# Optimization experiments

Hardware: AMD Instinct MI355X
Metric: run time of the kernel (lower is better)

## Reference

```python
import jax, jax.numpy as jnp
import numpy as np

DIM = 1024
N_HEADS = 16
HEAD_DIM = DIM // N_HEADS
HIDDEN = 4 * DIM
B, T = 4, 2048
EPS = 1e-5


def setup_inputs() -> dict:
    key = jax.random.key(0)
    ks = jax.random.split(key, 12)
    s = lambda fan_in: 1.0 / np.sqrt(fan_in)
    return {
        "x": jax.random.normal(ks[0], (B, T, DIM), jnp.float32),
        "ln1_g": jnp.ones((DIM,), jnp.float32),
        "ln1_b": jnp.zeros((DIM,), jnp.float32),
        "qkv_w": jax.random.normal(ks[1], (DIM, 3 * DIM), jnp.float32) * s(DIM),
        "qkv_b": jnp.zeros((3 * DIM,), jnp.float32),
        "proj_w": jax.random.normal(ks[2], (DIM, DIM), jnp.float32) * s(DIM),
        "proj_b": jnp.zeros((DIM,), jnp.float32),
        "ln2_g": jnp.ones((DIM,), jnp.float32),
        "ln2_b": jnp.zeros((DIM,), jnp.float32),
        "ff1_w": jax.random.normal(ks[3], (DIM, HIDDEN), jnp.float32) * s(DIM),
        "ff1_b": jnp.zeros((HIDDEN,), jnp.float32),
        "ff2_w": jax.random.normal(ks[4], (HIDDEN, DIM), jnp.float32) * s(HIDDEN),
        "ff2_b": jnp.zeros((DIM,), jnp.float32),
    }


def _layernorm(x, g, b):
    mu = jnp.mean(x, axis=-1, keepdims=True)
    var = jnp.mean(jnp.square(x - mu), axis=-1, keepdims=True)
    return (x - mu) * jax.lax.rsqrt(var + EPS) * g + b


def _attn(x, qkv_w, qkv_b, proj_w, proj_b):
    Bx, Tx, C = x.shape
    qkv = (x @ qkv_w + qkv_b).reshape(Bx, Tx, 3, N_HEADS, HEAD_DIM)
    q, k, v = (qkv[:, :, i].transpose(0, 2, 1, 3) for i in range(3))  # [B,H,T,hd]
    att = jnp.einsum('bhqd,bhkd->bhqk', q, k) / np.sqrt(HEAD_DIM)
    causal = jnp.tril(jnp.ones((Tx, Tx), bool))
    att = jnp.where(causal, att, -jnp.inf)
    att = jax.nn.softmax(att, axis=-1)
    out = jnp.einsum('bhqk,bhkd->bhqd', att, v).transpose(0, 2, 1, 3).reshape(Bx, Tx, C)
    return out @ proj_w + proj_b


def reference(x, ln1_g, ln1_b, qkv_w, qkv_b, proj_w, proj_b,
              ln2_g, ln2_b, ff1_w, ff1_b, ff2_w, ff2_b):
    x = x + _attn(_layernorm(x, ln1_g, ln1_b), qkv_w, qkv_b, proj_w, proj_b)
    h = _layernorm(x, ln2_g, ln2_b)
    h = jax.nn.gelu(h @ ff1_w + ff1_b, approximate=False) @ ff2_w + ff2_b
    return x + h
```

## Files before the change

### kernel.cpp

```cpp
#include <hip/hip_runtime.h>
#include <hip/hip_bf16.h>
#include <math.h>

#define DIM 1024
#define NHEADS 16
#define HD 64
#define TT 2048
#define BB 4
#define MTOK (BB*TT)
#define HID 4096

typedef __attribute__((ext_vector_type(8))) short bf16x8;
typedef __attribute__((ext_vector_type(4))) float f32x4;
typedef unsigned short u16;
typedef unsigned int u32;

__device__ inline u16 f2b(float f){
  __hip_bfloat16 h = __float2bfloat16(f);
  return __builtin_bit_cast(u16, h);
}

__device__ inline void load_lds16(const void* g, void* l){
  __builtin_amdgcn_global_load_lds(
      (const __attribute__((address_space(1))) void*)g,
      (__attribute__((address_space(3))) void*)l,
      16, 0, 0);
}

__global__ __launch_bounds__(256) void wconv_t(const float* __restrict__ W,
                                               u16* __restrict__ Wt, int K, int N){
  __shared__ float tl[32][33];
  const int k0 = blockIdx.x*32, n0 = blockIdx.y*32;
  const int tx = threadIdx.x & 31, ty = threadIdx.x >> 5;
  #pragma unroll
  for (int r=0;r<32;r+=8)
    tl[ty+r][tx] = W[(size_t)(k0+ty+r)*N + (n0+tx)];
  __syncthreads();
  #pragma unroll
  for (int r=0;r<32;r+=8)
    Wt[(size_t)(n0+ty+r)*K + (k0+tx)] = f2b(tl[tx][ty+r]);
}

__global__ __launch_bounds__(256) void ln_fwd(const float* __restrict__ x,
                                              const float* __restrict__ g,
                                              const float* __restrict__ bta,
                                              u16* __restrict__ out){
  const int row = blockIdx.x, t = threadIdx.x;
  const float4 v = ((const float4*)(x + (size_t)row*DIM))[t];
  float s  = v.x+v.y+v.z+v.w;
  float s2 = v.x*v.x+v.y*v.y+v.z*v.z+v.w*v.w;
  #pragma unroll
  for (int m=1;m<64;m<<=1){ s += __shfl_xor(s,m); s2 += __shfl_xor(s2,m); }
  __shared__ float red[8];
  if ((t&63)==0){ red[t>>6]=s; red[4+(t>>6)]=s2; }
  __syncthreads();
  s  = red[0]+red[1]+red[2]+red[3];
  s2 = red[4]+red[5]+red[6]+red[7];
  const float mu = s*(1.0f/DIM);
  const float rstd = rsqrtf(s2*(1.0f/DIM) - mu*mu + 1e-5f);
  const float4 gv = ((const float4*)g)[t];
  const float4 bv = ((const float4*)bta)[t];
  ushort4 ov;
  ov.x = f2b((v.x-mu)*rstd*gv.x + bv.x);
  ov.y = f2b((v.y-mu)*rstd*gv.y + bv.y);
  ov.z = f2b((v.z-mu)*rstd*gv.z + bv.z);
  ov.w = f2b((v.w-mu)*rstd*gv.w + bv.w);
  ((ushort4*)out)[(size_t)row*(DIM/4) + t] = ov;
}

template<int EPI>
__global__ __launch_bounds__(256) void gemm_bt(
    const u16* __restrict__ A, const u16* __restrict__ Bt,
    const float* __restrict__ bias, const float* __restrict__ resid,
    float* __restrict__ outf, u16* __restrict__ outh,
    u16* __restrict__ qo, u16* __restrict__ ko, u16* __restrict__ vo,
    int M, int N, int K)
{
  __shared__ __align__(16) u16 smem[16384];
  u16* As = smem;
  u16* Bs = smem + 8192;
  u16* Ct = smem;
  const int t = threadIdx.x, wv = t>>6, ln = t&63;
  const int nbx = gridDim.x, nwg = nbx*gridDim.y;
  const int bid = blockIdx.y*nbx + blockIdx.x;
  const int cpx = nwg>>3;
  const int wid = (bid&7)*cpx + (bid>>3);
  const int m0 = (wid/nbx)*128, n0 = (wid%nbx)*128;
  const int wr = wv>>1, wc = wv&1;
  const int hi = ln>>4, lr = hi*4, lc = ln&15;
  f32x4 acc[4][4] = {};

  int rdoff[2][2];
  #pragma unroll
  for (int kk=0; kk<2; kk++)
    rdoff[kk][0] = ((kk*4 + hi) ^ (lc&7)) << 3;

  for (int kt=0; kt<K; kt+=64){
    #pragma unroll
    for (int j=0;j<4;j++){
      const int chunk = j*256 + t;
      const int row = chunk>>3;
      const int cS  = (chunk&7) ^ (row&7);
      load_lds16(A  + (size_t)(m0+row)*K + kt + cS*8, (char*)As + chunk*16);
      load_lds16(Bt + (size_t)(n0+row)*K + kt + cS*8, (char*)Bs + chunk*16);
    }
    asm volatile("s_waitcnt vmcnt(0)" ::: "memory");
    __syncthreads();
    bf16x8 af[4][2], bfr[4][2];
    #pragma unroll
    for (int mi=0;mi<4;mi++){
      const int rbase = (wr*64 + mi*16 + lc) << 6;
      af[mi][0] = *(const bf16x8*)&As[rbase + rdoff[0][0]];
      af[mi][1] = *(const bf16x8*)&As[rbase + rdoff[1][0]];
    }
    #pragma unroll
    for (int ni=0;ni<4;ni++){
      const int rbase = (wc*64 + ni*16 + lc) << 6;
      bfr[ni][0] = *(const bf16x8*)&Bs[rbase + rdoff[0][0]];
      bfr[ni][1] = *(const bf16x8*)&Bs[rbase + rdoff[1][0]];
    }
    #pragma unroll
    for (int kk=0;kk<2;kk++)
      #pragma unroll
      for (int mi=0;mi<4;mi++)
        #pragma unroll
        for (int ni=0;ni<4;ni++)
          acc[mi][ni] = __builtin_amdgcn_mfma_f32_16x16x32_bf16(af[mi][kk], bfr[ni][kk], acc[mi][ni], 0,0,0);
    __syncthreads();
  }

  if constexpr (EPI==1 || EPI==3){
    #pragma unroll
    for (int ni=0;ni<4;ni++){
      const int gn = n0 + wc*64 + ni*16 + lc;
      const float bv = bias[gn];
      #pragma unroll
      for (int mi=0;mi<4;mi++){
        const int gmb = m0 + wr*64 + mi*16 + lr;
        f32x4 a = acc[mi][ni];
        #pragma unroll
        for (int i=0;i<4;i++){
          const size_t idx = (size_t)(gmb+i)*DIM + gn;
          outf[idx] = a[i] + bv + resid[idx];
        }
      }
    }
  } else {
    const int part = (EPI==0) ? (n0>>10) : 0;
    #pragma unroll
    for (int ni=0;ni<4;ni++){
      const int gn = n0 + wc*64 + ni*16 + lc;
      const float bv = bias[gn];
      const int cl = wc*64 + ni*16 + lc;
      #pragma unroll
      for (int mi=0;mi<4;mi++){
        f32x4 a = acc[mi][ni];
        #pragma unroll
        for (int i=0;i<4;i++){
          const int rl = wr*64 + mi*16 + lr + i;
          float val = a[i] + bv;
          if constexpr (EPI==2)
            val = 0.5f*val*(1.0f + erff(val*0.70710678118654752f));
          int r, c;
          if (EPI==0 && part==2){ r = cl; c = rl; } else { r = rl; c = cl; }
          const int chunk = c>>3;
          const int csw = (chunk&8) | ((chunk ^ (r&7)) & 7);
          Ct[(r<<7) + (csw<<3) + (c&7)] = f2b(val);
        }
      }
    }
    __syncthreads();
    const int cid = t & 7, rsub = t >> 3;
    const int bb = m0>>11, tok0b = m0&2047;
    const int h0 = (EPI==0) ? ((n0&1023)>>6) : 0;
    #pragma unroll
    for (int pass=0; pass<4; ++pass){
      const int rr = pass*32 + rsub;
      #pragma unroll
      for (int hh=0; hh<2; ++hh){
        const int chunk = hh*8 + cid;
        const int sw = (chunk&8) | ((chunk ^ (rr&7)) & 7);
        const bf16x8 vvv = *(const bf16x8*)&Ct[(rr<<7) + (sw<<3)];
        if constexpr (EPI==2){
          *(bf16x8*)&outh[(size_t)(m0+rr)*HID + n0 + chunk*8] = vvv;
        } else {
          if (part==2){
            const int head = h0 + (rr>>6), d = rr&63;
            *(bf16x8*)&vo[(((size_t)bb*NHEADS + head)*HD + d)*TT + tok0b + chunk*8] = vvv;
          } else {
            u16* dst = part ? ko : qo;
            const int head = h0 + hh;
            *(bf16x8*)&dst[(((size_t)bb*NHEADS + head)*TT + tok0b + rr)*HD + cid*8] = vvv;
          }
        }
      }
    }
  }
}

__global__ __launch_bounds__(512) void attn_fwd(
    const u16* __restrict__ qpt, const u16* __restrict__ kb, const u16* __restrict__ vtb,
    u16* __restrict__ o)
{
  __shared__ __align__(16) u16 Kd[2][64*64];
  __shared__ __align__(16) u16 Vd[2][64*64];
  __shared__ __align__(16) u32 Ps[8][16*40];
  const int t = threadIdx.x, wv = t>>6, ln = t&63;
  const int bid  = blockIdx.y*gridDim.x + blockIdx.x;
  const int orig = (bid&7)*128 + (bid>>3);
  const int bh   = orig>>4;
  const int qb   = 15 - (orig&15);
  const size_t base = (size_t)bh*TT*HD;
  const int hi = ln>>4, lc = ln&15;
  const int nt = 2*qb + 2;
  const int qbase = qb*128 + wv*16;
  const int qrow  = qbase + lc;

  const bf16x8 qf0 = *(const bf16x8*)(qpt + base + (size_t)qrow*HD + hi*8);
  const bf16x8 qf1 = *(const bf16x8*)(qpt + base + (size_t)qrow*HD + 32 + hi*8);
  f32x4 oacc[4] = {};
  float mrun = -1e30f, lrun = 0.f;
  const float SCQ = 0.125f * 1.44269504f;
  u32* pw = Ps[wv];

  const int srow = t>>3;
  const int sch  = t&7;
  const int gch  = (sch ^ (srow&7))<<3;

  auto STAGE = [&](int nb, int kt){
    load_lds16(kb  + base + (size_t)(kt*64+srow)*HD + gch, &Kd[nb][srow*64 + sch*8]);
    load_lds16(vtb + base + (size_t)srow*TT + kt*64 + gch, &Vd[nb][srow*64 + sch*8]);
  };
  auto FRAG = [&](const u16* buf, int r, int ch)->bf16x8{
    return *(const bf16x8*)(buf + r*64 + ((ch ^ (r&7))<<3));
  };

  int cur = 0;
  STAGE(0, 0);
  asm volatile("s_waitcnt vmcnt(0)" ::: "memory");
  __syncthreads();

  for (int kt=0; kt<nt; kt++){
    if (kt+1 < nt) STAGE(cur^1, kt+1);
    const u16* Kb = Kd[cur];
    const u16* Vb = Vd[cur];
    if (kt*64 <= qbase + 15){
      float p[4][4];
      float mx = -1e30f;
      __builtin_amdgcn_s_setprio(1);
      #pragma unroll
      for (int cf=0;cf<4;cf++){
        const int r = cf*16 + lc;
        const bf16x8 kf0 = FRAG(Kb, r, hi);
        const bf16x8 kf1 = FRAG(Kb, r, hi+4);
        f32x4 z = {0.f,0.f,0.f,0.f};
        z = __builtin_amdgcn_mfma_f32_16x16x32_bf16(kf0, qf0, z, 0,0,0);
        z = __builtin_amdgcn_mfma_f32_16x16x32_bf16(kf1, qf1, z, 0,0,0);
        p[cf][0]=z[0]; p[cf][1]=z[1]; p[cf][2]=z[2]; p[cf][3]=z[3];
      }
      __builtin_amdgcn_s_setprio(0);
      if (kt*64 + 63 > qbase){
        #pragma unroll
        for (int cf=0;cf<4;cf++)
          #pragma unroll
          for (int i=0;i<4;i++){
            const int kvg = kt*64 + cf*16 + 4*hi + i;
            float sv = p[cf][i]*SCQ;
            sv = (kvg > qrow) ? -1e30f : sv;
            p[cf][i] = sv;
            mx = fmaxf(mx, sv);
          }
      } else {
        #pragma unroll
        for (int cf=0;cf<4;cf++)
          #pragma unroll
          for (int i=0;i<4;i++){
            const float sv = p[cf][i]*SCQ;
            p[cf][i] = sv;
            mx = fmaxf(mx, sv);
          }
      }
      mx = fmaxf(mx, __shfl_xor(mx, 16));
      mx = fmaxf(mx, __shfl_xor(mx, 32));
      if (__any(mx > mrun + 11.0f)){
        const float mnew = fmaxf(mrun, mx);
        const float sc = exp2f(mrun - mnew);
        mrun = mnew;
        lrun *= sc;
        const float s0 = __shfl(sc, 4*hi+0);
        const float s1 = __shfl(sc, 4*hi+1);
        const float s2 = __shfl(sc, 4*hi+2);
        const float s3 = __shfl(sc, 4*hi+3);
        #pragma unroll
        for (int df=0;df<4;df++){
          oacc[df][0] *= s0; oacc[df][1] *= s1;
          oacc[df][2] *= s2; oacc[df][3] *= s3;
        }
      }
      float ssum = 0.f;
      #pragma unroll
      for (int cf=0;cf<4;cf++)
        #pragma unroll
        for (int i=0;i<4;i++){
          const float pv = exp2f(p[cf][i] - mrun);
          p[cf][i] = pv;
          ssum += pv;
        }
      ssum += __shfl_xor(ssum, 16);
      ssum += __shfl_xor(ssum, 32);
      lrun += ssum;
      #pragma unroll
      for (int cf=0;cf<4;cf++){
        uint2 wpk;
        wpk.x = (u32)f2b(p[cf][0]) | ((u32)f2b(p[cf][1])<<16);
        wpk.y = (u32)f2b(p[cf][2]) | ((u32)f2b(p[cf][3])<<16);
        *(uint2*)&pw[lc*40 + cf*8 + 2*hi] = wpk;
      }
      asm volatile("s_waitcnt lgkmcnt(0)" ::: "memory");
      __builtin_amdgcn_sched_barrier(0);
      const bf16x8 paA = *(const bf16x8*)&pw[lc*40 + 4*hi];
      const bf16x8 paB = *(const bf16x8*)&pw[lc*40 + 16 + 4*hi];
      __builtin_amdgcn_s_setprio(1);
      #pragma unroll
      for (int df=0;df<4;df++){
        const bf16x8 v0 = FRAG(Vb, df*16+lc, hi);
        const bf16x8 v1 = FRAG(Vb, df*16+lc, hi+4);
        oacc[df] = __builtin_amdgcn_mfma_f32_16x16x32_bf16(paA, v0, oacc[df], 0,0,0);
        oacc[df] = __builtin_amdgcn_mfma_f32_16x16x32_bf16(paB, v1, oacc[df], 0,0,0);
      }
      __builtin_amdgcn_s_setprio(0);
    }
    asm volatile("s_waitcnt vmcnt(0)" ::: "memory");
    __syncthreads();
    cur ^= 1;
  }

  const int b = bh>>4, h = bh&15;
  const float l0 = __shfl(lrun, 4*hi+0);
  const float l1 = __shfl(lrun, 4*hi+1);
  const float l2 = __shfl(lrun, 4*hi+2);
  const float l3 = __shfl(lrun, 4*hi+3);
  const float inv[4] = {1.0f/l0, 1.0f/l1, 1.0f/l2, 1.0f/l3};
  const int qg0 = qbase + 4*hi;
  #pragma unroll
  for (int i=0;i<4;i++){
    const size_t rowb = ((size_t)b*TT + (size_t)(qg0 + i))*DIM + h*HD;
    #pragma unroll
    for (int df=0;df<4;df++)
      o[rowb + df*16 + lc] = f2b(oacc[df][i]*inv[i]);
  }
}

extern "C" void kernel_launch(void* const* d_in, const int* in_sizes, int n_in,
                              void* d_out, int out_size, void* d_ws, size_t ws_size,
                              hipStream_t stream){
  (void)in_sizes; (void)n_in; (void)out_size; (void)ws_size;
  const float* x     = (const float*)d_in[0];
  const float* ln1g  = (const float*)d_in[1];
  const float* ln1b  = (const float*)d_in[2];
  const float* qkvw  = (const float*)d_in[3];
  const float* qkvb  = (const float*)d_in[4];
  const float* projw = (const float*)d_in[5];
  const float* projb = (const float*)d_in[6];
  const float* ln2g  = (const float*)d_in[7];
  const float* ln2b  = (const float*)d_in[8];
  const float* ff1w  = (const float*)d_in[9];
  const float* ff1b  = (const float*)d_in[10];
  const float* ff2w  = (const float*)d_in[11];
  const float* ff2b  = (const float*)d_in[12];
  float* out = (float*)d_out;

  char* ws = (char*)d_ws;
  size_t off = 0;
  auto alloc = [&](size_t n){ char* p = ws + off; off += (n + 255) & ~(size_t)255; return p; };
  u16* wqkvt  = (u16*)alloc((size_t)3072*1024*2);
  u16* wprojt = (u16*)alloc((size_t)1024*1024*2);
  u16* wff1t  = (u16*)alloc((size_t)4096*1024*2);
  u16* wff2t  = (u16*)alloc((size_t)1024*4096*2);
  u16* h1     = (u16*)alloc((size_t)MTOK*DIM*2);
  u16* qbuf   = (u16*)alloc((size_t)MTOK*DIM*2);
  u16* kbuf   = (u16*)alloc((size_t)MTOK*DIM*2);
  u16* vbuf   = (u16*)alloc((size_t)MTOK*DIM*2);
  u16* aout   = (u16*)alloc((size_t)MTOK*DIM*2);
  float* x2   = (float*)alloc((size_t)MTOK*DIM*4);
  u16* h2     = (u16*)alloc((size_t)MTOK*DIM*2);
  u16* act    = (u16*)alloc((size_t)MTOK*HID*2);

  wconv_t<<<dim3(1024/32, 3072/32), 256, 0, stream>>>(qkvw, wqkvt, 1024, 3072);
  wconv_t<<<dim3(1024/32, 1024/32), 256, 0, stream>>>(projw, wprojt, 1024, 1024);
  wconv_t<<<dim3(1024/32, 4096/32), 256, 0, stream>>>(ff1w, wff1t, 1024, 4096);
  wconv_t<<<dim3(4096/32, 1024/32), 256, 0, stream>>>(ff2w, wff2t, 4096, 1024);

  ln_fwd<<<MTOK, 256, 0, stream>>>(x, ln1g, ln1b, h1);

  gemm_bt<0><<<dim3(3072/128, MTOK/128), 256, 0, stream>>>(
      h1, wqkvt, qkvb, nullptr, nullptr, nullptr, qbuf, kbuf, vbuf, MTOK, 3072, 1024);

  attn_fwd<<<dim3(TT/128, BB*NHEADS), 512, 0, stream>>>(qbuf, kbuf, vbuf, aout);

  gemm_bt<1><<<dim3(1024/128, MTOK/128), 256, 0, stream>>>(
      aout, wprojt, projb, x, x2, nullptr, nullptr, nullptr, nullptr, MTOK, 1024, 1024);

  ln_fwd<<<MTOK, 256, 0, stream>>>(x2, ln2g, ln2b, h2);

  gemm_bt<2><<<dim3(4096/128, MTOK/128), 256, 0, stream>>>(
      h2, wff1t, ff1b, nullptr, nullptr, act, nullptr, nullptr, nullptr, MTOK, HID, 1024);

  gemm_bt<3><<<dim3(1024/128, MTOK/128), 256, 0, stream>>>(
      act, wff2t, ff2b, x2, out, nullptr, nullptr, nullptr, nullptr, MTOK, DIM, HID);
}
```

Baseline: 481.0 us.

## Double-buffer GEMM LDS tiles with BK=32 to overlap loads and MFMA

Restructures the GEMM main loop so K steps by 32, with two LDS buffers: the next tile's global→LDS loads are issued before computing on the current buffer, and one barrier per iteration replaces two. The XOR swizzle on the LDS layout is dropped in favour of a plain row-major 32-column layout. A barrier is added before the epilogue reuses shared memory. The smaller K tile doubles the iteration count and the unswizzled reads may cause LDS bank conflicts.

New measurement: 492.3 us. 1.02x slower.

```diff
diff --git a/kernel.cpp b/kernel.cpp
--- a/kernel.cpp
+++ b/kernel.cpp
@@ -77,8 +77,6 @@
     int M, int N, int K)
 {
   __shared__ __align__(16) u16 smem[16384];
-  u16* As = smem;
-  u16* Bs = smem + 8192;
   u16* Ct = smem;
   const int t = threadIdx.x, wv = t>>6, ln = t&63;
   const int nbx = gridDim.x, nwg = nbx*gridDim.y;
@@ -90,44 +88,49 @@
   const int hi = ln>>4, lr = hi*4, lc = ln&15;
   f32x4 acc[4][4] = {};
 
-  int rdoff[2][2];
-  #pragma unroll
-  for (int kk=0; kk<2; kk++)
-    rdoff[kk][0] = ((kk*4 + hi) ^ (lc&7)) << 3;
-
-  for (int kt=0; kt<K; kt+=64){
-    #pragma unroll
-    for (int j=0;j<4;j++){
-      const int chunk = j*256 + t;
-      const int row = chunk>>3;
-      const int cS  = (chunk&7) ^ (row&7);
-      load_lds16(A  + (size_t)(m0+row)*K + kt + cS*8, (char*)As + chunk*16);
-      load_lds16(Bt + (size_t)(n0+row)*K + kt + cS*8, (char*)Bs + chunk*16);
+  const int srow = t>>2;
+  const int sc16 = t&3;
+
+  auto STAGE = [&](int buf, int kt){
+    u16* As = smem + buf*8192;
+    u16* Bs = smem + buf*8192 + 4096;
+    #pragma unroll
+    for (int j=0;j<2;j++){
+      const int row = j*64 + srow;
+      load_lds16(A  + (size_t)(m0+row)*K + kt + sc16*8, (char*)As + (row*4 + sc16)*16);
+      load_lds16(Bt + (size_t)(n0+row)*K + kt + sc16*8, (char*)Bs + (row*4 + sc16)*16);
     }
+  };
+  auto COMPUTE = [&](int buf){
+    const u16* As = smem + buf*8192;
+    const u16* Bs = smem + buf*8192 + 4096;
+    bf16x8 af[4], bfr[4];
+    #pragma unroll
+    for (int mi=0;mi<4;mi++)
+      af[mi] = *(const bf16x8*)&As[(wr*64 + mi*16 + lc)*32 + hi*8];
+    #pragma unroll
+    for (int ni=0;ni<4;ni++)
+      bfr[ni] = *(const bf16x8*)&Bs[(wc*64 + ni*16 + lc)*32 + hi*8];
+    #pragma unroll
+    for (int mi=0;mi<4;mi++)
+      #pragma unroll
+      for (int ni=0;ni<4;ni++)
+        acc[mi][ni] = __builtin_amdgcn_mfma_f32_16x16x32_bf16(af[mi], bfr[ni], acc[mi][ni], 0,0,0);
+  };
+
+  const int nk = K>>5;
+  int cur = 0;
+  STAGE(0, 0);
+  asm volatile("s_waitcnt vmcnt(0)" ::: "memory");
+  __syncthreads();
+  for (int kt=1; kt<nk; ++kt){
+    STAGE(cur^1, kt<<5);
+    COMPUTE(cur);
     asm volatile("s_waitcnt vmcnt(0)" ::: "memory");
     __syncthreads();
-    bf16x8 af[4][2], bfr[4][2];
-    #pragma unroll
-    for (int mi=0;mi<4;mi++){
-      const int rbase = (wr*64 + mi*16 + lc) << 6;
-      af[mi][0] = *(const bf16x8*)&As[rbase + rdoff[0][0]];
-      af[mi][1] = *(const bf16x8*)&As[rbase + rdoff[1][0]];
-    }
-    #pragma unroll
-    for (int ni=0;ni<4;ni++){
-      const int rbase = (wc*64 + ni*16 + lc) << 6;
-      bfr[ni][0] = *(const bf16x8*)&Bs[rbase + rdoff[0][0]];
-      bfr[ni][1] = *(const bf16x8*)&Bs[rbase + rdoff[1][0]];
-    }
-    #pragma unroll
-    for (int kk=0;kk<2;kk++)
-      #pragma unroll
-      for (int mi=0;mi<4;mi++)
-        #pragma unroll
-        for (int ni=0;ni<4;ni++)
-          acc[mi][ni] = __builtin_amdgcn_mfma_f32_16x16x32_bf16(af[mi][kk], bfr[ni][kk], acc[mi][ni], 0,0,0);
-    __syncthreads();
+    cur ^= 1;
   }
+  COMPUTE(cur);
 
   if constexpr (EPI==1 || EPI==3){
     #pragma unroll
@@ -147,6 +150,7 @@
     }
   } else {
     const int part = (EPI==0) ? (n0>>10) : 0;
+    __syncthreads();
     #pragma unroll
     for (int ni=0;ni<4;ni++){
       const int gn = n0 + wc*64 + ni*16 + lc;
```

## Add 256x256-tile triple-buffered GEMM for QKV and FF1 projections

Applied to the files above, without the earlier changes.

Introduces a 512-thread GEMM kernel with 256x256 output tiles, BK=32 and a three-stage LDS ring of async global-to-LDS loads. Staging of later k-tiles is interleaved with MFMA quads and MFMA priority is raised, so loads can overlap compute. It is used for the QKV and FF1 GEMMs when 96KB of dynamic LDS can be enabled. Larger tiles raise arithmetic intensity per workgroup, at the cost of fewer workgroups, occupancy limited to one block per CU, and an epilogue that writes through LDS in four serialized chunks.

Result: slower. 578.9 us (+20.4%).

```diff
diff --git a/kernel.cpp b/kernel.cpp
--- a/kernel.cpp
+++ b/kernel.cpp
@@ -69,6 +69,144 @@
 }
 
 template<int EPI>
+__global__ __launch_bounds__(512) void gemm256(
+    const u16* __restrict__ A, const u16* __restrict__ Bt,
+    const float* __restrict__ bias, u16* __restrict__ outh,
+    u16* __restrict__ qo, u16* __restrict__ ko, u16* __restrict__ vo,
+    int K)
+{
+  extern __shared__ __align__(16) u16 smem[];
+  u16* Ct = smem;
+  const int t = threadIdx.x, wv = t>>6, ln = t&63;
+  const int nbx = gridDim.x, nwg = nbx*gridDim.y;
+  const int bid = blockIdx.y*nbx + blockIdx.x;
+  const int cpx = nwg>>3;
+  const int wid = (bid&7)*cpx + (bid>>3);
+  const int m0 = (wid/nbx)*256, n0 = (wid%nbx)*256;
+  const int wr = wv>>2, wc = wv&3;
+  const int hi = ln>>4, lc = ln&15;
+  f32x4 acc[8][4] = {};
+  bf16x8 bfr[4];
+
+  auto STAGE = [&](int buf, int kt, int which){
+    const u16* src = which ? Bt : A;
+    const int org = which ? n0 : m0;
+    u16* dstb = smem + buf*16384 + which*8192;
+    #pragma unroll
+    for (int j=0;j<2;j++){
+      const int chunk = j*512 + t;
+      const int row = chunk>>2, c = chunk&3;
+      const int cS = c ^ (row&3);
+      load_lds16(src + (size_t)(org+row)*K + kt*32 + cS*8, (char*)dstb + chunk*16);
+    }
+  };
+  auto QUAD = [&](int buf, int mih){
+    const u16* As_ = smem + buf*16384;
+    const u16* Bs_ = smem + buf*16384 + 8192;
+    if (mih==0){
+      #pragma unroll
+      for (int ni=0;ni<4;ni++){
+        const int r = wc*64 + ni*16 + lc;
+        bfr[ni] = *(const bf16x8*)&Bs_[r*32 + ((hi^(r&3))<<3)];
+      }
+    }
+    bf16x8 af[4];
+    #pragma unroll
+    for (int mi=0;mi<4;mi++){
+      const int r = wr*128 + (mih*4+mi)*16 + lc;
+      af[mi] = *(const bf16x8*)&As_[r*32 + ((hi^(r&3))<<3)];
+    }
+    __builtin_amdgcn_s_setprio(1);
+    #pragma unroll
+    for (int mi=0;mi<4;mi++)
+      #pragma unroll
+      for (int ni=0;ni<4;ni++)
+        acc[mih*4+mi][ni] = __builtin_amdgcn_mfma_f32_16x16x32_bf16(af[mi], bfr[ni], acc[mih*4+mi][ni], 0,0,0);
+    __builtin_amdgcn_s_setprio(0);
+  };
+
+  const int nkt = K>>5;
+  STAGE(0,0,0); STAGE(0,0,1);
+  STAGE(1,1,0); STAGE(1,1,1);
+  asm volatile("s_waitcnt vmcnt(4)" ::: "memory");
+  __syncthreads();
+
+  for (int tt=0; tt<nkt; ++tt){
+    const int bt_ = tt%3, bs_ = (tt+2)%3;
+    const bool st = (tt+2) < nkt;
+    if (st) STAGE(bs_, tt+2, 0);
+    QUAD(bt_, 0);
+    if (st) STAGE(bs_, tt+2, 1);
+    QUAD(bt_, 1);
+    if (tt+1 < nkt){
+      if (st) asm volatile("s_waitcnt vmcnt(4)" ::: "memory");
+      else    asm volatile("s_waitcnt vmcnt(0)" ::: "memory");
+      __syncthreads();
+    }
+  }
+
+  const int bb = m0>>11;
+  const int wch = wc&1;
+  #pragma unroll
+  for (int h=0;h<2;h++){
+    #pragma unroll
+    for (int ch=0;ch<2;ch++){
+      const int part = (EPI==0) ? ((n0 + ch*128)>>10) : 0;
+      const int h0 = ((n0 + ch*128)&1023)>>6;
+      __syncthreads();
+      if (wr==h && (wc>>1)==ch){
+        #pragma unroll
+        for (int ni=0;ni<4;ni++){
+          const int gn = n0 + wc*64 + ni*16 + lc;
+          const float bv = bias[gn];
+          const int cl = wch*64 + ni*16 + lc;
+          #pragma unroll
+          for (int mi=0;mi<8;mi++){
+            f32x4 a = acc[mi][ni];
+            #pragma unroll
+            for (int i=0;i<4;i++){
+              const int rl = mi*16 + hi*4 + i;
+              float val = a[i] + bv;
+              if constexpr (EPI==2)
+                val = 0.5f*val*(1.0f + erff(val*0.70710678118654752f));
+              int r = rl, c = cl;
+              if (EPI==0 && part==2){ r = cl; c = rl; }
+              const int chunk = c>>3;
+              const int csw = (chunk&8) | ((chunk ^ (r&7)) & 7);
+              Ct[(r<<7) + (csw<<3) + (c&7)] = f2b(val);
+            }
+          }
+        }
+      }
+      __syncthreads();
+      const int cid = t&7, rsub = t>>3;
+      const int tok0b = (m0&2047) + h*128;
+      #pragma unroll
+      for (int p=0;p<2;p++){
+        const int rr = p*64 + rsub;
+        #pragma unroll
+        for (int hh=0;hh<2;hh++){
+          const int chunk = hh*8 + cid;
+          const int sw = (chunk&8) | ((chunk ^ (rr&7)) & 7);
+          const bf16x8 vvv = *(const bf16x8*)&Ct[(rr<<7) + (sw<<3)];
+          if constexpr (EPI==2){
+            *(bf16x8*)&outh[(size_t)(m0 + h*128 + rr)*HID + n0 + ch*128 + chunk*8] = vvv;
+          } else {
+            if (part==2){
+              const int head = h0 + (rr>>6), d = rr&63;
+              *(bf16x8*)&vo[(((size_t)bb*NHEADS + head)*HD + d)*TT + tok0b + chunk*8] = vvv;
+            } else {
+              u16* dst = part ? ko : qo;
+              *(bf16x8*)&dst[(((size_t)bb*NHEADS + h0 + hh)*TT + tok0b + rr)*HD + cid*8] = vvv;
+            }
+          }
+        }
+      }
+    }
+  }
+}
+
+template<int EPI>
 __global__ __launch_bounds__(256) void gemm_bt(
     const u16* __restrict__ A, const u16* __restrict__ Bt,
     const float* __restrict__ bias, const float* __restrict__ resid,
@@ -90,10 +228,10 @@
   const int hi = ln>>4, lr = hi*4, lc = ln&15;
   f32x4 acc[4][4] = {};
 
-  int rdoff[2][2];
+  int rdoff[2];
   #pragma unroll
   for (int kk=0; kk<2; kk++)
-    rdoff[kk][0] = ((kk*4 + hi) ^ (lc&7)) << 3;
+    rdoff[kk] = ((kk*4 + hi) ^ (lc&7)) << 3;
 
   for (int kt=0; kt<K; kt+=64){
     #pragma unroll
@@ -110,14 +248,14 @@
     #pragma unroll
     for (int mi=0;mi<4;mi++){
       const int rbase = (wr*64 + mi*16 + lc) << 6;
-      af[mi][0] = *(const bf16x8*)&As[rbase + rdoff[0][0]];
-      af[mi][1] = *(const bf16x8*)&As[rbase + rdoff[1][0]];
+      af[mi][0] = *(const bf16x8*)&As[rbase + rdoff[0]];
+      af[mi][1] = *(const bf16x8*)&As[rbase + rdoff[1]];
     }
     #pragma unroll
     for (int ni=0;ni<4;ni++){
       const int rbase = (wc*64 + ni*16 + lc) << 6;
-      bfr[ni][0] = *(const bf16x8*)&Bs[rbase + rdoff[0][0]];
-      bfr[ni][1] = *(const bf16x8*)&Bs[rbase + rdoff[1][0]];
+      bfr[ni][0] = *(const bf16x8*)&Bs[rbase + rdoff[0]];
+      bfr[ni][1] = *(const bf16x8*)&Bs[rbase + rdoff[1]];
     }
     #pragma unroll
     for (int kk=0;kk<2;kk++)
@@ -147,6 +285,7 @@
     }
   } else {
     const int part = (EPI==0) ? (n0>>10) : 0;
+    __syncthreads();
     #pragma unroll
     for (int ni=0;ni<4;ni++){
       const int gn = n0 + wc*64 + ni*16 + lc;
@@ -161,8 +300,8 @@
           float val = a[i] + bv;
           if constexpr (EPI==2)
             val = 0.5f*val*(1.0f + erff(val*0.70710678118654752f));
-          int r, c;
-          if (EPI==0 && part==2){ r = cl; c = rl; } else { r = rl; c = cl; }
+          int r = rl, c = cl;
+          if (EPI==0 && part==2){ r = cl; c = rl; }
           const int chunk = c>>3;
           const int csw = (chunk&8) | ((chunk ^ (r&7)) & 7);
           Ct[(r<<7) + (csw<<3) + (c&7)] = f2b(val);
@@ -386,6 +525,12 @@
   u16* h2     = (u16*)alloc((size_t)MTOK*DIM*2);
   u16* act    = (u16*)alloc((size_t)MTOK*HID*2);
 
+  hipError_t eA = hipFuncSetAttribute(reinterpret_cast<const void*>(&gemm256<0>),
+                                      hipFuncAttributeMaxDynamicSharedMemorySize, 98304);
+  hipError_t eB = hipFuncSetAttribute(reinterpret_cast<const void*>(&gemm256<2>),
+                                      hipFuncAttributeMaxDynamicSharedMemorySize, 98304);
+  const bool big = (eA == hipSuccess) && (eB == hipSuccess);
+
   wconv_t<<<dim3(1024/32, 3072/32), 256, 0, stream>>>(qkvw, wqkvt, 1024, 3072);
   wconv_t<<<dim3(1024/32, 1024/32), 256, 0, stream>>>(projw, wprojt, 1024, 1024);
   wconv_t<<<dim3(1024/32, 4096/32), 256, 0, stream>>>(ff1w, wff1t, 1024, 4096);
@@ -393,8 +538,12 @@
 
   ln_fwd<<<MTOK, 256, 0, stream>>>(x, ln1g, ln1b, h1);
 
-  gemm_bt<0><<<dim3(3072/128, MTOK/128), 256, 0, stream>>>(
-      h1, wqkvt, qkvb, nullptr, nullptr, nullptr, qbuf, kbuf, vbuf, MTOK, 3072, 1024);
+  if (big)
+    gemm256<0><<<dim3(3072/256, MTOK/256), 512, 98304, stream>>>(
+        h1, wqkvt, qkvb, nullptr, qbuf, kbuf, vbuf, 1024);
+  else
+    gemm_bt<0><<<dim3(3072/128, MTOK/128), 256, 0, stream>>>(
+        h1, wqkvt, qkvb, nullptr, nullptr, nullptr, qbuf, kbuf, vbuf, MTOK, 3072, 1024);
 
   attn_fwd<<<dim3(TT/128, BB*NHEADS), 512, 0, stream>>>(qbuf, kbuf, vbuf, aout);
 
@@ -403,8 +552,12 @@
 
   ln_fwd<<<MTOK, 256, 0, stream>>>(x2, ln2g, ln2b, h2);
 
-  gemm_bt<2><<<dim3(4096/128, MTOK/128), 256, 0, stream>>>(
-      h2, wff1t, ff1b, nullptr, nullptr, act, nullptr, nullptr, nullptr, MTOK, HID, 1024);
+  if (big)
+    gemm256<2><<<dim3(4096/256, MTOK/256), 512, 98304, stream>>>(
+        h2, wff1t, ff1b, act, nullptr, nullptr, nullptr, 1024);
+  else
+    gemm_bt<2><<<dim3(4096/128, MTOK/128), 256, 0, stream>>>(
+        h2, wff1t, ff1b, nullptr, nullptr, act, nullptr, nullptr, nullptr, MTOK, HID, 1024);
 
   gemm_bt<3><<<dim3(1024/128, MTOK/128), 256, 0, stream>>>(
       act, wff2t, ff2b, x2, out, nullptr, nullptr, nullptr, nullptr, MTOK, DIM, HID);
```

## Keep attention P in registers via shuffles and compute row sums with MFMA

Applied to the files above, without the earlier changes.

The attention kernel no longer writes the bf16 probability tile to LDS and reads it back. It packs values with v_cvt_pk_bf16_f32 and rearranges them into MFMA A-operand layout with cross-lane shuffles. Row sums are accumulated by an extra MFMA against a vector of ones instead of scalar adds and shuffle reductions. The FF1 GELU epilogue swaps erff for an exp2/rcp sigmoid-style approximation, and a barrier is added before the epilogue's LDS reuse. The GELU change carries accuracy risk, and the shuffles add VALU work in place of the LDS traffic.

Measured after the change: 464.2 us. 3.5% less time.

```diff
diff --git a/kernel.cpp b/kernel.cpp
--- a/kernel.cpp
+++ b/kernel.cpp
@@ -18,6 +18,12 @@
 __device__ inline u16 f2b(float f){
   __hip_bfloat16 h = __float2bfloat16(f);
   return __builtin_bit_cast(u16, h);
+}
+
+__device__ inline u32 cvtpk(float lo, float hi_){
+  u32 r;
+  asm("v_cvt_pk_bf16_f32 %0, %1, %2" : "=v"(r) : "v"(lo), "v"(hi_));
+  return r;
 }
 
 __device__ inline void load_lds16(const void* g, void* l){
@@ -90,10 +96,10 @@
   const int hi = ln>>4, lr = hi*4, lc = ln&15;
   f32x4 acc[4][4] = {};
 
-  int rdoff[2][2];
+  int rdoff[2];
   #pragma unroll
   for (int kk=0; kk<2; kk++)
-    rdoff[kk][0] = ((kk*4 + hi) ^ (lc&7)) << 3;
+    rdoff[kk] = ((kk*4 + hi) ^ (lc&7)) << 3;
 
   for (int kt=0; kt<K; kt+=64){
     #pragma unroll
@@ -110,14 +116,14 @@
     #pragma unroll
     for (int mi=0;mi<4;mi++){
       const int rbase = (wr*64 + mi*16 + lc) << 6;
-      af[mi][0] = *(const bf16x8*)&As[rbase + rdoff[0][0]];
-      af[mi][1] = *(const bf16x8*)&As[rbase + rdoff[1][0]];
+      af[mi][0] = *(const bf16x8*)&As[rbase + rdoff[0]];
+      af[mi][1] = *(const bf16x8*)&As[rbase + rdoff[1]];
     }
     #pragma unroll
     for (int ni=0;ni<4;ni++){
       const int rbase = (wc*64 + ni*16 + lc) << 6;
-      bfr[ni][0] = *(const bf16x8*)&Bs[rbase + rdoff[0][0]];
-      bfr[ni][1] = *(const bf16x8*)&Bs[rbase + rdoff[1][0]];
+      bfr[ni][0] = *(const bf16x8*)&Bs[rbase + rdoff[0]];
+      bfr[ni][1] = *(const bf16x8*)&Bs[rbase + rdoff[1]];
     }
     #pragma unroll
     for (int kk=0;kk<2;kk++)
@@ -147,6 +153,7 @@
     }
   } else {
     const int part = (EPI==0) ? (n0>>10) : 0;
+    __syncthreads();
     #pragma unroll
     for (int ni=0;ni<4;ni++){
       const int gn = n0 + wc*64 + ni*16 + lc;
@@ -159,10 +166,15 @@
         for (int i=0;i<4;i++){
           const int rl = wr*64 + mi*16 + lr + i;
           float val = a[i] + bv;
-          if constexpr (EPI==2)
-            val = 0.5f*val*(1.0f + erff(val*0.70710678118654752f));
-          int r, c;
-          if (EPI==0 && part==2){ r = cl; c = rl; } else { r = rl; c = cl; }
+          if constexpr (EPI==2){
+            const float xx = val*val;
+            const float w  = val * fmaf(xx, 0.10294322f, 2.30220781f);
+            const float y  = exp2f(w);
+            const float r_ = __builtin_amdgcn_rcpf(1.0f + y);
+            val = val - val*r_;
+          }
+          int r = rl, c = cl;
+          if (EPI==0 && part==2){ r = cl; c = rl; }
           const int chunk = c>>3;
           const int csw = (chunk&8) | ((chunk ^ (r&7)) & 7);
           Ct[(r<<7) + (csw<<3) + (c&7)] = f2b(val);
@@ -204,7 +216,6 @@
 {
   __shared__ __align__(16) u16 Kd[2][64*64];
   __shared__ __align__(16) u16 Vd[2][64*64];
-  __shared__ __align__(16) u32 Ps[8][16*40];
   const int t = threadIdx.x, wv = t>>6, ln = t&63;
   const int bid  = blockIdx.y*gridDim.x + blockIdx.x;
   const int orig = (bid&7)*128 + (bid>>3);
@@ -219,9 +230,12 @@
   const bf16x8 qf0 = *(const bf16x8*)(qpt + base + (size_t)qrow*HD + hi*8);
   const bf16x8 qf1 = *(const bf16x8*)(qpt + base + (size_t)qrow*HD + 32 + hi*8);
   f32x4 oacc[4] = {};
-  float mrun = -1e30f, lrun = 0.f;
+  f32x4 lsum = {0.f,0.f,0.f,0.f};
+  float mrun = -1e30f;
   const float SCQ = 0.125f * 1.44269504f;
-  u32* pw = Ps[wv];
+  bf16x8 ones;
+  #pragma unroll
+  for (int j=0;j<8;j++) ones[j] = (short)0x3F80;
 
   const int srow = t>>3;
   const int sch  = t&7;
@@ -234,6 +248,13 @@
   auto FRAG = [&](const u16* buf, int r, int ch)->bf16x8{
     return *(const bf16x8*)(buf + r*64 + ((ch ^ (r&7))<<3));
   };
+  const int src0 = ((ln&16)<<1) + lc;
+  const int src1 = src0 + 16;
+  auto pick = [&](u32 w0, u32 w1, int src)->u32{
+    const u32 a = (u32)__shfl((int)w0, src);
+    const u32 b = (u32)__shfl((int)w1, src);
+    return (hi<2) ? a : b;
+  };
 
   int cur = 0;
   STAGE(0, 0);
@@ -245,8 +266,7 @@
     const u16* Kb = Kd[cur];
     const u16* Vb = Vd[cur];
     if (kt*64 <= qbase + 15){
-      float p[4][4];
-      float mx = -1e30f;
+      float sv[4][4];
       __builtin_amdgcn_s_setprio(1);
       #pragma unroll
       for (int cf=0;cf<4;cf++){
@@ -256,28 +276,29 @@
         f32x4 z = {0.f,0.f,0.f,0.f};
         z = __builtin_amdgcn_mfma_f32_16x16x32_bf16(kf0, qf0, z, 0,0,0);
         z = __builtin_amdgcn_mfma_f32_16x16x32_bf16(kf1, qf1, z, 0,0,0);
-        p[cf][0]=z[0]; p[cf][1]=z[1]; p[cf][2]=z[2]; p[cf][3]=z[3];
+        sv[cf][0]=z[0]; sv[cf][1]=z[1]; sv[cf][2]=z[2]; sv[cf][3]=z[3];
       }
       __builtin_amdgcn_s_setprio(0);
+      float mx = -1e30f;
       if (kt*64 + 63 > qbase){
         #pragma unroll
         for (int cf=0;cf<4;cf++)
           #pragma unroll
           for (int i=0;i<4;i++){
             const int kvg = kt*64 + cf*16 + 4*hi + i;
-            float sv = p[cf][i]*SCQ;
-            sv = (kvg > qrow) ? -1e30f : sv;
-            p[cf][i] = sv;
-            mx = fmaxf(mx, sv);
+            float s_ = sv[cf][i]*SCQ;
+            s_ = (kvg > qrow) ? -1e30f : s_;
+            sv[cf][i] = s_;
+            mx = fmaxf(mx, s_);
           }
       } else {
         #pragma unroll
         for (int cf=0;cf<4;cf++)
           #pragma unroll
           for (int i=0;i<4;i++){
-            const float sv = p[cf][i]*SCQ;
-            p[cf][i] = sv;
-            mx = fmaxf(mx, sv);
+            const float s_ = sv[cf][i]*SCQ;
+            sv[cf][i] = s_;
+            mx = fmaxf(mx, s_);
           }
       }
       mx = fmaxf(mx, __shfl_xor(mx, 16));
@@ -286,7 +307,6 @@
         const float mnew = fmaxf(mrun, mx);
         const float sc = exp2f(mrun - mnew);
         mrun = mnew;
-        lrun *= sc;
         const float s0 = __shfl(sc, 4*hi+0);
         const float s1 = __shfl(sc, 4*hi+1);
         const float s2 = __shfl(sc, 4*hi+2);
@@ -296,30 +316,29 @@
           oacc[df][0] *= s0; oacc[df][1] *= s1;
           oacc[df][2] *= s2; oacc[df][3] *= s3;
         }
-      }
-      float ssum = 0.f;
-      #pragma unroll
-      for (int cf=0;cf<4;cf++)
-        #pragma unroll
-        for (int i=0;i<4;i++){
-          const float pv = exp2f(p[cf][i] - mrun);
-          p[cf][i] = pv;
-          ssum += pv;
-        }
-      ssum += __shfl_xor(ssum, 16);
-      ssum += __shfl_xor(ssum, 32);
-      lrun += ssum;
+        lsum[0] *= s0; lsum[1] *= s1; lsum[2] *= s2; lsum[3] *= s3;
+      }
+      u32 W[4][2];
       #pragma unroll
       for (int cf=0;cf<4;cf++){
-        uint2 wpk;
-        wpk.x = (u32)f2b(p[cf][0]) | ((u32)f2b(p[cf][1])<<16);
-        wpk.y = (u32)f2b(p[cf][2]) | ((u32)f2b(p[cf][3])<<16);
-        *(uint2*)&pw[lc*40 + cf*8 + 2*hi] = wpk;
-      }
-      asm volatile("s_waitcnt lgkmcnt(0)" ::: "memory");
-      __builtin_amdgcn_sched_barrier(0);
-      const bf16x8 paA = *(const bf16x8*)&pw[lc*40 + 4*hi];
-      const bf16x8 paB = *(const bf16x8*)&pw[lc*40 + 16 + 4*hi];
+        const float e0 = exp2f(sv[cf][0] - mrun);
+        const float e1 = exp2f(sv[cf][1] - mrun);
+        const float e2 = exp2f(sv[cf][2] - mrun);
+        const float e3 = exp2f(sv[cf][3] - mrun);
+        W[cf][0] = cvtpk(e0, e1);
+        W[cf][1] = cvtpk(e2, e3);
+      }
+      uint4 uA, uB;
+      uA.x = pick(W[0][0], W[1][0], src0);
+      uA.y = pick(W[0][1], W[1][1], src0);
+      uA.z = pick(W[0][0], W[1][0], src1);
+      uA.w = pick(W[0][1], W[1][1], src1);
+      uB.x = pick(W[2][0], W[3][0], src0);
+      uB.y = pick(W[2][1], W[3][1], src0);
+      uB.z = pick(W[2][0], W[3][0], src1);
+      uB.w = pick(W[2][1], W[3][1], src1);
+      const bf16x8 paA = __builtin_bit_cast(bf16x8, uA);
+      const bf16x8 paB = __builtin_bit_cast(bf16x8, uB);
       __builtin_amdgcn_s_setprio(1);
       #pragma unroll
       for (int df=0;df<4;df++){
@@ -328,6 +347,8 @@
         oacc[df] = __builtin_amdgcn_mfma_f32_16x16x32_bf16(paA, v0, oacc[df], 0,0,0);
         oacc[df] = __builtin_amdgcn_mfma_f32_16x16x32_bf16(paB, v1, oacc[df], 0,0,0);
       }
+      lsum = __builtin_amdgcn_mfma_f32_16x16x32_bf16(paA, ones, lsum, 0,0,0);
+      lsum = __builtin_amdgcn_mfma_f32_16x16x32_bf16(paB, ones, lsum, 0,0,0);
       __builtin_amdgcn_s_setprio(0);
     }
     asm volatile("s_waitcnt vmcnt(0)" ::: "memory");
@@ -336,11 +357,7 @@
   }
 
   const int b = bh>>4, h = bh&15;
-  const float l0 = __shfl(lrun, 4*hi+0);
-  const float l1 = __shfl(lrun, 4*hi+1);
-  const float l2 = __shfl(lrun, 4*hi+2);
-  const float l3 = __shfl(lrun, 4*hi+3);
-  const float inv[4] = {1.0f/l0, 1.0f/l1, 1.0f/l2, 1.0f/l3};
+  const float inv[4] = {1.0f/lsum[0], 1.0f/lsum[1], 1.0f/lsum[2], 1.0f/lsum[3]};
   const int qg0 = qbase + 4*hi;
   #pragma unroll
   for (int i=0;i<4;i++){
```
